# Kernel tuning notes

Hardware: AMD Instinct MI355X
Metric: run time of the kernel (lower is better)

The kernel has to match this reference:

```python
import jax, jax.numpy as jnp
import numpy as np

B = 16384
C = 1000  # num_classes
H = 128   # adapter hidden


def setup_inputs() -> dict:
    key = jax.random.key(0)
    k1, k2, k3 = jax.random.split(key, 3)
    logits = jax.random.normal(k1, (B, C), dtype=jnp.float32)
    # adapter_net params: Linear(C->H) -> ReLU -> Linear(H->C); stored as x @ W + b
    W1 = jax.random.normal(k2, (C, H), dtype=jnp.float32) * 0.03
    b1 = jnp.zeros((H,), dtype=jnp.float32)
    W2 = jax.random.normal(k3, (H, C), dtype=jnp.float32) * 0.03
    b2 = jnp.zeros((C,), dtype=jnp.float32)
    return {"logits": logits, "W1": W1, "b1": b1, "W2": W2, "b2": b2}


def reference(logits, W1, b1, W2, b2):
    prob = jax.nn.softmax(logits, axis=-1)                       # [B, C]
    # descending sort
    order = jnp.argsort(-prob, axis=-1)                          # [B, C] int
    sorted_prob = jnp.take_along_axis(prob, order, axis=-1)      # [B, C]
    # diffs between consecutive sorted probs, last column = 1
    diffs = jnp.concatenate(
        [sorted_prob[:, :-1] - sorted_prob[:, 1:],
         jnp.ones((prob.shape[0], 1), dtype=prob.dtype)], axis=-1)
    # adapter net on prob
    h = jax.nn.relu(prob @ W1 + b1)                              # [B, H]
    cal = h @ W2 + b2                                            # [B, C]
    cal = jnp.concatenate([jax.nn.sigmoid(cal[:, :-1]), cal[:, -1:]], axis=-1)
    c = diffs * cal                                              # [B, C]
    # U @ c  (U upper-triangular ones) == reverse cumulative sum along last dim
    rev_cumsum = jnp.cumsum(c[:, ::-1], axis=-1)[:, ::-1]        # [B, C]
    # S.T @ v scatters sorted-position values back to original class positions
    inv_order = jnp.argsort(order, axis=-1)                      # inverse permutation
    fitted = jnp.take_along_axis(rev_cumsum, inv_order, axis=-1)
    return fitted + logits
```

## Files before the change

kernel.cpp:

```cpp
#include <hip/hip_runtime.h>
#include <hip/hip_bf16.h>
#include <math.h>

#define B_ROWS 16384
#define C_CLS  1000
#define H_DIM  128
#define NEG_BIG (-3.0e38f)

#define MT    16
#define PSTR  1064
#define CSTR  1064
#define HSTR  136
#define KT1   32
#define CT1   8
#define KT2   4
#define CT2   64
#define SLICE 576

#define QSCALE 511.0f
#define QINV   (1.0f / 511.0f)

typedef __attribute__((ext_vector_type(8))) short short8;
typedef __attribute__((ext_vector_type(4))) float f32x4;

__device__ __forceinline__ unsigned short f2bf(float x) {
    unsigned int u = __float_as_uint(x);
    unsigned int r = (u + 0x7FFFu + ((u >> 16) & 1u)) >> 16;
    return (unsigned short)r;
}
__device__ __forceinline__ float bf2f(unsigned short v) {
    return __uint_as_float(((unsigned int)v) << 16);
}
__device__ __forceinline__ float sigm(float x) {
    return 1.0f / (1.0f + __expf(-x));
}
__device__ __forceinline__ unsigned int umin(unsigned int a, unsigned int b) {
    return a < b ? a : b;
}
__device__ __forceinline__ int SKU(int i) { return i + (i >> 4); }
__device__ __forceinline__ int PSL(unsigned int b) {
    return (int)((b >> 3) + (b & 7u) * 68u);
}

__global__ __launch_bounds__(256) void pack_kernel(
    const float* __restrict__ W1, const float* __restrict__ W2,
    unsigned short* __restrict__ W1p, unsigned short* __restrict__ W2p)
{
    const int t = blockIdx.x * 256 + threadIdx.x;
    if (t < 16384) {
        const int lane = t & 63, slot = t >> 6;
        const int kt = slot >> 3, ct = slot & 7;
        const int col = ct * 16 + (lane & 15);
        const int k0 = kt * 32 + (lane >> 4) * 8;
        unsigned short v[8];
        #pragma unroll
        for (int j = 0; j < 8; ++j) {
            int k = k0 + j;
            v[j] = f2bf((k < C_CLS) ? W1[k * H_DIM + col] : 0.f);
        }
        #pragma unroll
        for (int j = 0; j < 8; ++j) W1p[(size_t)t * 8 + j] = v[j];
    } else {
        const int t2 = t - 16384;
        const int lane = t2 & 63, slot = t2 >> 6;
        const int kt = slot >> 6, ct = slot & 63;
        const int col = ct * 16 + (lane & 15);
        const int k0 = kt * 32 + (lane >> 4) * 8;
        unsigned short v[8];
        #pragma unroll
        for (int j = 0; j < 8; ++j) {
            int k = k0 + j;
            v[j] = f2bf((col < C_CLS) ? W2[k * C_CLS + col] : 0.f);
        }
        #pragma unroll
        for (int j = 0; j < 8; ++j) W2p[(size_t)t2 * 8 + j] = v[j];
    }
}

__global__ __launch_bounds__(512) void fused_kernel(
    const float* __restrict__ logits, const float* __restrict__ bias1,
    const float* __restrict__ bias2, const unsigned short* __restrict__ W1p,
    const unsigned short* __restrict__ W2p, float* __restrict__ out)
{
    __shared__ alignas(16) unsigned short probS[MT * PSTR];
    __shared__ alignas(16) unsigned int uniReg[8 * 2 * SLICE];
    __shared__ float qsA[MT], svsA[MT], rowInv[MT], rowLast[MT];

    unsigned short* calS = probS;
    unsigned short* hS = (unsigned short*)uniReg;

    const int tid = threadIdx.x;
    const int w = tid >> 6, lane = tid & 63;
    const size_t row0 = (size_t)blockIdx.x * MT;

    #pragma unroll
    for (int rr = 0; rr < 2; ++rr) {
        const int r = 2 * w + rr;
        const float* lr = logits + (row0 + r) * C_CLS;
        float sum = 0.f, mx = NEG_BIG;
        for (int c4 = lane; c4 < 250; c4 += 64) {
            const float4 x = reinterpret_cast<const float4*>(lr)[c4];
            float e0 = __expf(x.x), e1 = __expf(x.y);
            float e2 = __expf(x.z), e3 = __expf(x.w);
            sum += (e0 + e1) + (e2 + e3);
            mx = fmaxf(mx, fmaxf(fmaxf(x.x, x.y), fmaxf(x.z, x.w)));
            uint2 pk;
            asm("v_cvt_pk_bf16_f32 %0, %1, %2" : "=v"(pk.x) : "v"(e0), "v"(e1));
            asm("v_cvt_pk_bf16_f32 %0, %1, %2" : "=v"(pk.y) : "v"(e2), "v"(e3));
            *reinterpret_cast<uint2*>(&probS[r * PSTR + 4 * c4]) = pk;
        }
        #pragma unroll
        for (int off = 32; off; off >>= 1) {
            sum += __shfl_xor(sum, off);
            mx = fmaxf(mx, __shfl_xor(mx, off));
        }
        if (lane == 0) {
            const float maxe = __expf(mx);
            rowInv[r] = 1.0f / sum;
            qsA[r]  = QSCALE / maxe;
            svsA[r] = maxe * QINV * (1.0f / sum);
        }
        if (lane < 12) *reinterpret_cast<unsigned int*>(&probS[r * PSTR + 1000 + 2 * lane]) = 0u;
    }
    __syncthreads();

    {
        f32x4 acc = {0.f, 0.f, 0.f, 0.f};
        const unsigned short* aptr = probS + (lane & 15) * PSTR + (lane >> 4) * 8;
        #pragma unroll 4
        for (int kt = 0; kt < KT1; ++kt) {
            short8 a = *reinterpret_cast<const short8*>(aptr + kt * 32);
            short8 b = *reinterpret_cast<const short8*>(W1p + ((size_t)(kt * CT1 + w) * 64 + lane) * 8);
            acc = __builtin_amdgcn_mfma_f32_16x16x32_bf16(a, b, acc, 0, 0, 0);
        }
        const int hc = w * 16 + (lane & 15);
        const float bb = bias1[hc];
        #pragma unroll
        for (int i = 0; i < 4; ++i) {
            const int hrow = (lane >> 4) * 4 + i;
            hS[hrow * HSTR + hc] = f2bf(fmaxf(acc[i] * rowInv[hrow] + bb, 0.f));
        }
    }

    unsigned int dP[2][8];
    #pragma unroll
    for (int rr = 0; rr < 2; ++rr) {
        const int r = 2 * w + rr;
        const float qs = qsA[r];
        #pragma unroll
        for (int k = 0; k < 8; ++k) {
            const unsigned int pk =
                *reinterpret_cast<const unsigned int*>(&probS[r * PSTR + 2 * lane + 128 * k]);
            unsigned int d0 = umin((unsigned int)(bf2f((unsigned short)(pk & 0xFFFFu)) * qs), 511u);
            unsigned int d1 = umin((unsigned int)(bf2f((unsigned short)(pk >> 16)) * qs), 511u);
            dP[rr][k] = d0 | (d1 << 16);
        }
    }
    __syncthreads();

    {
        f32x4 acc[8];
        #pragma unroll
        for (int t = 0; t < 8; ++t) acc[t] = (f32x4){0.f, 0.f, 0.f, 0.f};
        const unsigned short* haptr = hS + (lane & 15) * HSTR + (lane >> 4) * 8;
        #pragma unroll
        for (int kt = 0; kt < KT2; ++kt) {
            short8 a = *reinterpret_cast<const short8*>(haptr + kt * 32);
            #pragma unroll
            for (int t = 0; t < 8; ++t) {
                short8 b = *reinterpret_cast<const short8*>(
                    W2p + ((size_t)(kt * CT2 + 8 * w + t) * 64 + lane) * 8);
                acc[t] = __builtin_amdgcn_mfma_f32_16x16x32_bf16(a, b, acc[t], 0, 0, 0);
            }
        }
        #pragma unroll
        for (int t = 0; t < 8; ++t) {
            const int col = (8 * w + t) * 16 + (lane & 15);
            if (col < C_CLS) {
                const int sc = SKU(col);
                #pragma unroll
                for (int i = 0; i < 4; ++i) {
                    const int rloc = (lane >> 4) * 4 + i;
                    float v = acc[t][i] + bias2[col];
                    calS[rloc * CSTR + sc] = f2bf(v);
                    if (col == C_CLS - 1) rowLast[rloc] = v;
                }
            }
        }
    }
    __syncthreads();

    unsigned int* hist0 = uniReg + (size_t)w * 2 * SLICE;
    unsigned int* hist1 = hist0 + SLICE;
    float* Pb0 = (float*)hist0;
    float* Pb1 = (float*)hist1;
    const bool act7 = lane < 52;
    const size_t rowbase0 = (row0 + 2 * w) * C_CLS;
    const size_t rowbase1 = rowbase0 + C_CLS;

    float2 xf[2][8];
    #pragma unroll
    for (int k = 0; k < 8; ++k) {
        if (k < 7 || act7) {
            xf[0][k] = *reinterpret_cast<const float2*>(&logits[rowbase0 + 2 * lane + 128 * k]);
            xf[1][k] = *reinterpret_cast<const float2*>(&logits[rowbase1 + 2 * lane + 128 * k]);
        }
    }

    #pragma unroll
    for (int k = 0; k < 4; ++k) {
        hist0[64 * k + lane] = 0u;
        hist1[64 * k + lane] = 0u;
    }

    #pragma unroll
    for (int k = 0; k < 8; ++k) {
        if (k < 7 || act7) {
            const unsigned int a0 = dP[0][k] & 0xFFFFu, a1 = dP[0][k] >> 16;
            atomicAdd(&hist0[a0 >> 1], 1u << ((a0 & 1u) * 16u));
            atomicAdd(&hist0[a1 >> 1], 1u << ((a1 & 1u) * 16u));
            const unsigned int b0 = dP[1][k] & 0xFFFFu, b1 = dP[1][k] >> 16;
            atomicAdd(&hist1[b0 >> 1], 1u << ((b0 & 1u) * 16u));
            atomicAdd(&hist1[b1 >> 1], 1u << ((b1 & 1u) * 16u));
        }
    }

    unsigned int c[2][8], T[2];
    #pragma unroll
    for (int rr = 0; rr < 2; ++rr) {
        uint4 v = *reinterpret_cast<uint4*>(&(rr ? hist1 : hist0)[4 * lane]);
        c[rr][0] = v.x & 0xFFFFu; c[rr][1] = v.x >> 16;
        c[rr][2] = v.y & 0xFFFFu; c[rr][3] = v.y >> 16;
        c[rr][4] = v.z & 0xFFFFu; c[rr][5] = v.z >> 16;
        c[rr][6] = v.w & 0xFFFFu; c[rr][7] = v.w >> 16;
        T[rr] = ((c[rr][0] + c[rr][1]) + (c[rr][2] + c[rr][3]))
              + ((c[rr][4] + c[rr][5]) + (c[rr][6] + c[rr][7]));
    }

    unsigned int base0_[2];
    int prev_[2];
    {
        unsigned int x0 = T[0], x1 = T[1];
        int h0 = -1, h1 = -1;
        #pragma unroll
        for (int j = 0; j < 8; ++j) {
            if (c[0][j] > 0) h0 = 8 * lane + j;
            if (c[1][j] > 0) h1 = 8 * lane + j;
        }
        int m0 = h0, m1 = h1;
        #pragma unroll
        for (int off = 1; off < 64; off <<= 1) {
            unsigned int y0 = __shfl_up(x0, off);
            unsigned int y1 = __shfl_up(x1, off);
            int n0 = __shfl_up(m0, off);
            int n1 = __shfl_up(m1, off);
            if (lane >= off) { x0 += y0; x1 += y1; m0 = max(m0, n0); m1 = max(m1, n1); }
        }
        base0_[0] = x0 - T[0];
        base0_[1] = x1 - T[1];
        prev_[0] = __shfl_up(m0, 1);
        prev_[1] = __shfl_up(m1, 1);
        if (lane == 0) { prev_[0] = -1; prev_[1] = -1; }
    }

    float s[2][8], run_[2];
    #pragma unroll
    for (int rr = 0; rr < 2; ++rr) {
        const int r = 2 * w + rr;
        const float svs = svsA[r];
        unsigned int brun = base0_[rr];
        int prev = prev_[rr];
        float run = 0.f;
        #pragma unroll
        for (int j = 0; j < 8; ++j) {
            const int b = 8 * lane + j;
            float e = 0.f;
            if (c[rr][j] > 0) {
                if (brun == 0) {
                    e = rowLast[r];
                } else {
                    const float cl = bf2f(calS[r * CSTR + SKU((C_CLS - 1) - (int)brun)]);
                    e = (float)(b - prev) * svs * sigm(cl);
                }
                prev = b;
            }
            brun += c[rr][j];
            run += e;
            s[rr][j] = run;
        }
        run_[rr] = run;
    }

    float X_[2];
    {
        float x0 = run_[0], x1 = run_[1];
        #pragma unroll
        for (int off = 1; off < 64; off <<= 1) {
            float y0 = __shfl_up(x0, off);
            float y1 = __shfl_up(x1, off);
            if (lane >= off) { x0 += y0; x1 += y1; }
        }
        X_[0] = x0 - run_[0];
        X_[1] = x1 - run_[1];
    }

    #pragma unroll
    for (int j = 0; j < 8; ++j) {
        Pb0[lane + 68 * j] = X_[0] + s[0][j];
        Pb1[lane + 68 * j] = X_[1] + s[1][j];
    }

    #pragma unroll
    for (int k = 0; k < 8; ++k) {
        if (k < 7 || act7) {
            const int idx = 2 * lane + 128 * k;
            float2 ov0, ov1;
            ov0.x = Pb0[PSL(dP[0][k] & 0xFFFFu)] + xf[0][k].x;
            ov0.y = Pb0[PSL(dP[0][k] >> 16)] + xf[0][k].y;
            ov1.x = Pb1[PSL(dP[1][k] & 0xFFFFu)] + xf[1][k].x;
            ov1.y = Pb1[PSL(dP[1][k] >> 16)] + xf[1][k].y;
            *reinterpret_cast<float2*>(&out[rowbase0 + idx]) = ov0;
            *reinterpret_cast<float2*>(&out[rowbase1 + idx]) = ov1;
        }
    }
}

extern "C" void kernel_launch(void* const* d_in, const int* in_sizes, int n_in,
                              void* d_out, int out_size, void* d_ws, size_t ws_size,
                              hipStream_t stream)
{
    const float* logits = (const float*)d_in[0];
    const float* W1     = (const float*)d_in[1];
    const float* b1     = (const float*)d_in[2];
    const float* W2     = (const float*)d_in[3];
    const float* b2     = (const float*)d_in[4];
    float* out = (float*)d_out;

    unsigned short* W1p = (unsigned short*)d_ws;
    unsigned short* W2p = W1p + (size_t)KT1 * CT1 * 64 * 8;

    pack_kernel<<<dim3(128), dim3(256), 0, stream>>>(W1, W2, W1p, W2p);

    fused_kernel<<<dim3(B_ROWS / MT), dim3(512), 0, stream>>>(
        logits, b1, b2, W1p, W2p, out);
}
```

Before: 65.11 us.

## Halve rows per block to 8 with 4 waves, reuse LDS and drop logits prefetch

Each block now handles 8 rows with 256 threads instead of 16 rows with 512, and launch bounds request 4 blocks per CU. Each wave computes two hidden column tiles in the first GEMM and two passes in the second. Half of each 16-row MFMA tile is now wasted. The prefix buffers now reuse the probS rows with an XOR swizzle instead of a separate slice, and the histogram region shrinks. Logits are reloaded right before output instead of being held in registers. Together this shrinks LDS and register use to raise occupancy, at the cost of idle MFMA rows and a later global reload.

```diff
diff --git a/kernel.cpp b/kernel.cpp
--- a/kernel.cpp
+++ b/kernel.cpp
@@ -7,7 +7,7 @@
 #define H_DIM  128
 #define NEG_BIG (-3.0e38f)
 
-#define MT    16
+#define MT    8
 #define PSTR  1064
 #define CSTR  1064
 #define HSTR  136
@@ -15,7 +15,6 @@
 #define CT1   8
 #define KT2   4
 #define CT2   64
-#define SLICE 576
 
 #define QSCALE 511.0f
 #define QINV   (1.0f / 511.0f)
@@ -38,8 +37,8 @@
     return a < b ? a : b;
 }
 __device__ __forceinline__ int SKU(int i) { return i + (i >> 4); }
-__device__ __forceinline__ int PSL(unsigned int b) {
-    return (int)((b >> 3) + (b & 7u) * 68u);
+__device__ __forceinline__ int PSL2(unsigned int b) {
+    return (int)(((b >> 3) ^ ((b & 7u) << 3)) + (b & 7u) * 64u);
 }
 
 __global__ __launch_bounds__(256) void pack_kernel(
@@ -77,13 +76,13 @@
     }
 }
 
-__global__ __launch_bounds__(512) void fused_kernel(
+__global__ __launch_bounds__(256, 4) void fused_kernel(
     const float* __restrict__ logits, const float* __restrict__ bias1,
     const float* __restrict__ bias2, const unsigned short* __restrict__ W1p,
     const unsigned short* __restrict__ W2p, float* __restrict__ out)
 {
     __shared__ alignas(16) unsigned short probS[MT * PSTR];
-    __shared__ alignas(16) unsigned int uniReg[8 * 2 * SLICE];
+    __shared__ alignas(16) unsigned int uniReg[2048];
     __shared__ float qsA[MT], svsA[MT], rowInv[MT], rowLast[MT];
 
     unsigned short* calS = probS;
@@ -125,20 +124,26 @@
     __syncthreads();
 
     {
-        f32x4 acc = {0.f, 0.f, 0.f, 0.f};
-        const unsigned short* aptr = probS + (lane & 15) * PSTR + (lane >> 4) * 8;
+        f32x4 acc0 = {0.f, 0.f, 0.f, 0.f}, acc1 = {0.f, 0.f, 0.f, 0.f};
+        const unsigned short* aptr = probS + (lane & 7) * PSTR + (lane >> 4) * 8;
         #pragma unroll 4
         for (int kt = 0; kt < KT1; ++kt) {
             short8 a = *reinterpret_cast<const short8*>(aptr + kt * 32);
-            short8 b = *reinterpret_cast<const short8*>(W1p + ((size_t)(kt * CT1 + w) * 64 + lane) * 8);
-            acc = __builtin_amdgcn_mfma_f32_16x16x32_bf16(a, b, acc, 0, 0, 0);
-        }
-        const int hc = w * 16 + (lane & 15);
-        const float bb = bias1[hc];
+            short8 b0 = *reinterpret_cast<const short8*>(W1p + ((size_t)(kt * CT1 + 2 * w) * 64 + lane) * 8);
+            short8 b1 = *reinterpret_cast<const short8*>(W1p + ((size_t)(kt * CT1 + 2 * w + 1) * 64 + lane) * 8);
+            acc0 = __builtin_amdgcn_mfma_f32_16x16x32_bf16(a, b0, acc0, 0, 0, 0);
+            acc1 = __builtin_amdgcn_mfma_f32_16x16x32_bf16(a, b1, acc1, 0, 0, 0);
+        }
+        const int hc0 = 2 * w * 16 + (lane & 15);
+        const float bb0 = bias1[hc0], bb1 = bias1[hc0 + 16];
         #pragma unroll
         for (int i = 0; i < 4; ++i) {
             const int hrow = (lane >> 4) * 4 + i;
-            hS[hrow * HSTR + hc] = f2bf(fmaxf(acc[i] * rowInv[hrow] + bb, 0.f));
+            if (hrow < MT) {
+                const float s = rowInv[hrow];
+                hS[hrow * HSTR + hc0]      = f2bf(fmaxf(acc0[i] * s + bb0, 0.f));
+                hS[hrow * HSTR + hc0 + 16] = f2bf(fmaxf(acc1[i] * s + bb1, 0.f));
+            }
         }
     }
 
@@ -158,54 +163,48 @@
     }
     __syncthreads();
 
-    {
+    #pragma unroll
+    for (int p = 0; p < 2; ++p) {
         f32x4 acc[8];
         #pragma unroll
         for (int t = 0; t < 8; ++t) acc[t] = (f32x4){0.f, 0.f, 0.f, 0.f};
-        const unsigned short* haptr = hS + (lane & 15) * HSTR + (lane >> 4) * 8;
+        const unsigned short* haptr = hS + (lane & 7) * HSTR + (lane >> 4) * 8;
         #pragma unroll
         for (int kt = 0; kt < KT2; ++kt) {
             short8 a = *reinterpret_cast<const short8*>(haptr + kt * 32);
             #pragma unroll
             for (int t = 0; t < 8; ++t) {
                 short8 b = *reinterpret_cast<const short8*>(
-                    W2p + ((size_t)(kt * CT2 + 8 * w + t) * 64 + lane) * 8);
+                    W2p + ((size_t)(kt * CT2 + 16 * w + 8 * p + t) * 64 + lane) * 8);
                 acc[t] = __builtin_amdgcn_mfma_f32_16x16x32_bf16(a, b, acc[t], 0, 0, 0);
             }
         }
         #pragma unroll
         for (int t = 0; t < 8; ++t) {
-            const int col = (8 * w + t) * 16 + (lane & 15);
+            const int col = (16 * w + 8 * p + t) * 16 + (lane & 15);
             if (col < C_CLS) {
                 const int sc = SKU(col);
                 #pragma unroll
                 for (int i = 0; i < 4; ++i) {
                     const int rloc = (lane >> 4) * 4 + i;
-                    float v = acc[t][i] + bias2[col];
-                    calS[rloc * CSTR + sc] = f2bf(v);
-                    if (col == C_CLS - 1) rowLast[rloc] = v;
+                    if (rloc < MT) {
+                        float v = acc[t][i] + bias2[col];
+                        calS[rloc * CSTR + sc] = f2bf(v);
+                        if (col == C_CLS - 1) rowLast[rloc] = v;
+                    }
                 }
             }
         }
     }
     __syncthreads();
 
-    unsigned int* hist0 = uniReg + (size_t)w * 2 * SLICE;
-    unsigned int* hist1 = hist0 + SLICE;
-    float* Pb0 = (float*)hist0;
-    float* Pb1 = (float*)hist1;
+    unsigned int* hist0 = uniReg + w * 512;
+    unsigned int* hist1 = hist0 + 256;
+    float* Pb0 = (float*)&probS[(2 * w) * PSTR];
+    float* Pb1 = (float*)&probS[(2 * w + 1) * PSTR];
     const bool act7 = lane < 52;
     const size_t rowbase0 = (row0 + 2 * w) * C_CLS;
     const size_t rowbase1 = rowbase0 + C_CLS;
-
-    float2 xf[2][8];
-    #pragma unroll
-    for (int k = 0; k < 8; ++k) {
-        if (k < 7 || act7) {
-            xf[0][k] = *reinterpret_cast<const float2*>(&logits[rowbase0 + 2 * lane + 128 * k]);
-            xf[1][k] = *reinterpret_cast<const float2*>(&logits[rowbase1 + 2 * lane + 128 * k]);
-        }
-    }
 
     #pragma unroll
     for (int k = 0; k < 4; ++k) {
@@ -306,19 +305,22 @@
 
     #pragma unroll
     for (int j = 0; j < 8; ++j) {
-        Pb0[lane + 68 * j] = X_[0] + s[0][j];
-        Pb1[lane + 68 * j] = X_[1] + s[1][j];
+        const int slot = (int)((lane ^ (j << 3)) + 64 * j);
+        Pb0[slot] = X_[0] + s[0][j];
+        Pb1[slot] = X_[1] + s[1][j];
     }
 
     #pragma unroll
     for (int k = 0; k < 8; ++k) {
         if (k < 7 || act7) {
             const int idx = 2 * lane + 128 * k;
+            const float2 xf0 = *reinterpret_cast<const float2*>(&logits[rowbase0 + idx]);
+            const float2 xf1 = *reinterpret_cast<const float2*>(&logits[rowbase1 + idx]);
             float2 ov0, ov1;
-            ov0.x = Pb0[PSL(dP[0][k] & 0xFFFFu)] + xf[0][k].x;
-            ov0.y = Pb0[PSL(dP[0][k] >> 16)] + xf[0][k].y;
-            ov1.x = Pb1[PSL(dP[1][k] & 0xFFFFu)] + xf[1][k].x;
-            ov1.y = Pb1[PSL(dP[1][k] >> 16)] + xf[1][k].y;
+            ov0.x = Pb0[PSL2(dP[0][k] & 0xFFFFu)] + xf0.x;
+            ov0.y = Pb0[PSL2(dP[0][k] >> 16)] + xf0.y;
+            ov1.x = Pb1[PSL2(dP[1][k] & 0xFFFFu)] + xf1.x;
+            ov1.y = Pb1[PSL2(dP[1][k] >> 16)] + xf1.y;
             *reinterpret_cast<float2*>(&out[rowbase0 + idx]) = ov0;
             *reinterpret_cast<float2*>(&out[rowbase1 + idx]) = ov1;
         }
@@ -341,6 +343,6 @@
 
     pack_kernel<<<dim3(128), dim3(256), 0, stream>>>(W1, W2, W1p, W2p);
 
-    fused_kernel<<<dim3(B_ROWS / MT), dim3(512), 0, stream>>>(
+    fused_kernel<<<dim3(B_ROWS / MT), dim3(256), 0, stream>>>(
         logits, b1, b2, W1p, W2p, out);
 }
```

Result: slower. 92.33 us (+41.8%).
